# Kernel tuning notes

Measured on AMD Instinct MI355X. Metric: run time of the kernel, lower is better.

Reference implementation:

```python
import jax, jax.numpy as jnp
import numpy as np

B, SQ, SKV, D = 4, 4096, 4096, 64

def setup_inputs() -> dict:
    key = jax.random.key(0)
    kq, kv = jax.random.split(key)
    query = jax.random.normal(kq, (B, SQ, D), dtype=jnp.float32)
    value = jax.random.normal(kv, (B, SKV, D), dtype=jnp.float32)
    return {"query": query, "value": value}

def reference(query, value):
    # scores = Q @ V^T  (value acts as both keys and values; no 1/sqrt(d) scaling)
    scores = jnp.einsum('bqd,bkd->bqk', query, value)  # [B, SQ, SKV]
    dist = jax.nn.softmax(scores, axis=-1)
    context = jnp.einsum('bqk,bkd->bqd', dist, value)  # [B, SQ, D]
    return context
```

## Files before the change

### kernel.cpp

```cpp
#include <hip/hip_runtime.h>


#define NB   4
#define SQ   4096
#define SKV  4096
#define DH   64
#define L2E  1.44269504088896340736f

typedef _Float16 half8 __attribute__((ext_vector_type(8)));
typedef _Float16 half4 __attribute__((ext_vector_type(4)));
typedef _Float16 half2v __attribute__((ext_vector_type(2)));
typedef float f32x4 __attribute__((ext_vector_type(4)));
typedef unsigned short u16;

#define MFMA16(a, b, c) __builtin_amdgcn_mfma_f32_16x16x16f16((a), (b), (c), 0, 0, 0)
#define MFMA32(a, b, c) __builtin_amdgcn_mfma_f32_16x16x32_f16((a), (b), (c), 0, 0, 0)

__device__ __forceinline__ u16 f2h(float f) {
  _Float16 h = (_Float16)f;
  return __builtin_bit_cast(u16, h);
}
__device__ __forceinline__ half2v pkrtz(float a, float b) {
  return __builtin_bit_cast(half2v, __builtin_amdgcn_cvt_pkrtz(a, b));
}

typedef __attribute__((address_space(1))) void gvoid;
typedef __attribute__((address_space(3))) void lvoid;
__device__ __forceinline__ void dma16(const u16* g, u16* l) {
  __builtin_amdgcn_global_load_lds((gvoid*)g, (lvoid*)l, 16, 0, 0);
}

__global__ __launch_bounds__(256) void prep_kernel(
    const float* __restrict__ V, u16* __restrict__ vh, u16* __restrict__ vt) {
  __shared__ u16 ldsT[16 * 72];
  int blk = blockIdx.x;
  int b   = blk >> 8;
  int rem = blk & 255;
  int j0  = (rem >> 2) << 6;
  int d0  = (rem & 3) << 4;
  int t   = threadIdx.x;
  int j   = t >> 2;
  int dc  = (t & 3) << 2;

  const float* src = V + ((size_t)(b * SKV) + j0 + j) * DH + d0 + dc;
  float4 v4 = *(const float4*)src;
  u16 h[4] = {f2h(v4.x), f2h(v4.y), f2h(v4.z), f2h(v4.w)};
  unsigned p0 = (unsigned)h[0] | ((unsigned)h[1] << 16);
  unsigned p1 = (unsigned)h[2] | ((unsigned)h[3] << 16);
  int dfull = d0 + dc;
  int physd = ((((dfull >> 3) ^ (j & 7)) << 3)) + (dfull & 7);
  *(uint2*)(vh + ((size_t)(b * SKV) + j0 + j) * DH + physd) = make_uint2(p0, p1);

#pragma unroll
  for (int k = 0; k < 4; ++k) ldsT[(dc + k) * 72 + j] = h[k];
  __syncthreads();

  int dl = t >> 4;
  int jc = (t & 15) << 2;
  u16 tr[4];
#pragma unroll
  for (int k = 0; k < 4; ++k) tr[k] = ldsT[dl * 72 + jc + k];
  unsigned q0 = (unsigned)tr[0] | ((unsigned)tr[1] << 16);
  unsigned q1 = (unsigned)tr[2] | ((unsigned)tr[3] << 16);
  int d   = d0 + dl;
  int kc2 = jc >> 5;
  int g   = (jc >> 4) & 1;
  int qd  = (jc >> 2) & 3;
  int hp  = ((kc2 << 2) | qd) ^ (d & 7);
  *(uint2*)(vt + ((size_t)(b * DH) + d) * SKV + j0 + (hp << 3) + (g << 2)) =
      make_uint2(q0, q1);
}

__global__ __launch_bounds__(256, 4) void attn_kernel(
    const float* __restrict__ Q,
    const u16* __restrict__ vh,
    const u16* __restrict__ vt,
    u16* __restrict__ po,
    float* __restrict__ pm,
    float* __restrict__ pl,
    int S, int kvLen) {
  __shared__ __align__(16) u16 lds[2][2][4096];

  int blk  = blockIdx.x;
  int tile = blk / S;
  int s    = blk - tile * S;
  int b    = tile >> 6;
  int q0   = (tile & 63) << 6;
  int kv0  = s * kvLen;
  int t    = threadIdx.x;
  int wave = t >> 6;
  int lane = t & 63;
  int col  = lane & 15;
  int quad = lane >> 4;
  int qw   = q0 + (wave << 4);
  int c7   = col & 7;

  const u16* gv  = vh + (size_t)(b * SKV) * DH;
  const u16* gvt = vt + (size_t)(b * DH) * SKV;

  int r0 = t >> 3;
  int c0 = (t & 7) << 3;
  int wb = wave << 9;

  half8 qf[2];
#pragma unroll
  for (int kc = 0; kc < 2; ++kc) {
    const float* qp = Q + ((size_t)(b * SQ) + qw + col) * DH + kc * 32 + (quad << 3);
    float4 a0 = *(const float4*)qp;
    float4 a1 = *(const float4*)(qp + 4);
    half8 hq;
    hq[0] = (_Float16)(a0.x * L2E); hq[1] = (_Float16)(a0.y * L2E);
    hq[2] = (_Float16)(a0.z * L2E); hq[3] = (_Float16)(a0.w * L2E);
    hq[4] = (_Float16)(a1.x * L2E); hq[5] = (_Float16)(a1.y * L2E);
    hq[6] = (_Float16)(a1.z * L2E); hq[7] = (_Float16)(a1.w * L2E);
    qf[kc] = hq;
  }

  f32x4 o[4];
#pragma unroll
  for (int nf = 0; nf < 4; ++nf) o[nf] = (f32x4){0.f, 0.f, 0.f, 0.f};
  float m_r = -1e30f, l_r = 0.f;

  dma16(gv + ((size_t)(kv0 + r0) << 6) + c0,       &lds[0][0][0] + wb);
  dma16(gv + ((size_t)(kv0 + r0 + 32) << 6) + c0,  &lds[0][0][0] + 2048 + wb);
  dma16(gvt + (size_t)r0 * SKV + kv0 + c0,         &lds[0][1][0] + wb);
  dma16(gvt + (size_t)(r0 + 32) * SKV + kv0 + c0,  &lds[0][1][0] + 2048 + wb);

  int nIter = kvLen >> 6;
  int cur = 0;
  for (int it = 0; it < nIter; ++it) {
    __syncthreads();

    if ((it + 1) < nIter) {
      int j0n = kv0 + ((it + 1) << 6);
      u16* dv  = &lds[cur ^ 1][0][0];
      u16* dvt = &lds[cur ^ 1][1][0];
      dma16(gv + ((size_t)(j0n + r0) << 6) + c0,      dv + wb);
      dma16(gv + ((size_t)(j0n + r0 + 32) << 6) + c0, dv + 2048 + wb);
      dma16(gvt + (size_t)r0 * SKV + j0n + c0,        dvt + wb);
      dma16(gvt + (size_t)(r0 + 32) * SKV + j0n + c0, dvt + 2048 + wb);
    }

    const u16* sv = &lds[cur][0][0];
    const u16* st = &lds[cur][1][0];

    f32x4 sf[4];
#pragma unroll
    for (int nf = 0; nf < 4; ++nf) sf[nf] = (f32x4){0.f, 0.f, 0.f, 0.f};
#pragma unroll
    for (int nf = 0; nf < 4; ++nf) {
#pragma unroll
      for (int kc = 0; kc < 2; ++kc) {
        int ch = ((kc << 2) | quad) ^ c7;
        half8 av = *(const half8*)(sv + ((nf * 16 + col) << 6) + (ch << 3));
        sf[nf] = MFMA32(av, qf[kc], sf[nf]);
      }
    }

    half4 pf[4];
    {
      float tm = sf[0][0];
#pragma unroll
      for (int nf = 0; nf < 4; ++nf)
#pragma unroll
        for (int r = 0; r < 4; ++r) tm = fmaxf(tm, sf[nf][r]);
      tm = fmaxf(tm, __shfl_xor(tm, 16, 64));
      tm = fmaxf(tm, __shfl_xor(tm, 32, 64));
      float mn = fmaxf(m_r, tm);
      float al = exp2f(m_r - mn);
      m_r = mn;
      float rs = 0.f;
#pragma unroll
      for (int nf = 0; nf < 4; ++nf) {
        float p0 = exp2f(sf[nf][0] - mn);
        float p1 = exp2f(sf[nf][1] - mn);
        float p2 = exp2f(sf[nf][2] - mn);
        float p3 = exp2f(sf[nf][3] - mn);
        rs += (p0 + p1) + (p2 + p3);
        half2v lo = pkrtz(p0, p1);
        half2v hi = pkrtz(p2, p3);
        pf[nf] = __builtin_shufflevector(lo, hi, 0, 1, 2, 3);
      }
      l_r = l_r * al + rs;
#pragma unroll
      for (int nf = 0; nf < 4; ++nf)
#pragma unroll
        for (int r = 0; r < 4; ++r) o[nf][r] *= al;
    }

#pragma unroll
    for (int kc2 = 0; kc2 < 2; ++kc2) {
#pragma unroll
      for (int nf2 = 0; nf2 < 4; ++nf2) {
        int ch = ((kc2 << 2) | quad) ^ c7;
        half8 w8 = *(const half8*)(st + ((nf2 * 16 + col) << 6) + (ch << 3));
        half4 wlo = __builtin_shufflevector(w8, w8, 0, 1, 2, 3);
        half4 whi = __builtin_shufflevector(w8, w8, 4, 5, 6, 7);
        o[nf2] = MFMA16(wlo, pf[kc2 * 2], o[nf2]);
        o[nf2] = MFMA16(whi, pf[kc2 * 2 + 1], o[nf2]);
      }
    }

    cur ^= 1;
  }

  l_r += __shfl_xor(l_r, 16, 64);
  l_r += __shfl_xor(l_r, 32, 64);
  int pidx = tile * S + s;
  if (quad == 0) {
    pm[(size_t)pidx * 64 + (wave << 4) + col] = m_r;
    pl[(size_t)pidx * 64 + (wave << 4) + col] = l_r;
  }

  __syncthreads();
  u16* tp = &lds[0][0][0];
  {
    int qrow = (wave << 4) + col;
#pragma unroll
    for (int nf2 = 0; nf2 < 4; ++nf2) {
#pragma unroll
      for (int r2 = 0; r2 < 4; r2 += 2) {
        unsigned pk = (unsigned)f2h(o[nf2][r2]) |
                      ((unsigned)f2h(o[nf2][r2 + 1]) << 16);
        int d = nf2 * 16 + (quad << 2) + r2;
        *(unsigned*)(tp + qrow * 72 + d) = pk;
      }
    }
  }
  __syncthreads();
  {
    u16* pob = po + (size_t)pidx * 64 * 64;
    int q = t >> 2, hc = (t & 3) << 4;
    uint4 x0 = *(const uint4*)(tp + q * 72 + hc);
    uint4 x1 = *(const uint4*)(tp + q * 72 + hc + 8);
    *(uint4*)(pob + q * 64 + hc)     = x0;
    *(uint4*)(pob + q * 64 + hc + 8) = x1;
  }
}

__global__ __launch_bounds__(256) void combine_kernel(
    const u16* __restrict__ po,
    const float* __restrict__ pm,
    const float* __restrict__ pl,
    float* __restrict__ out, int S) {
  int t    = threadIdx.x;
  int rowg = blockIdx.x * 32 + (t >> 3);
  int tile = rowg >> 6;
  int row  = rowg & 63;
  int dc   = (t & 7) << 3;

  float mv[8], lv[8];
  float M = -1e30f;
  for (int s = 0; s < S; ++s) {
    mv[s] = pm[(size_t)(tile * S + s) * 64 + row];
    lv[s] = pl[(size_t)(tile * S + s) * 64 + row];
    M = fmaxf(M, mv[s]);
  }
  float L = 0.f, w[8];
  for (int s = 0; s < S; ++s) {
    w[s] = exp2f(mv[s] - M);
    L += lv[s] * w[s];
  }
  float acc[8] = {0.f, 0.f, 0.f, 0.f, 0.f, 0.f, 0.f, 0.f};
  for (int s = 0; s < S; ++s) {
    const u16* p = po + (size_t)(tile * S + s) * 4096 + row * 64 + dc;
    uint4 raw = *(const uint4*)p;
    half8 x = __builtin_bit_cast(half8, raw);
#pragma unroll
    for (int k = 0; k < 8; ++k) acc[k] += w[s] * (float)x[k];
  }
  float invL = 1.0f / L;
  float* op = out + (size_t)rowg * 64 + dc;
  f32x4 o0 = (f32x4){acc[0], acc[1], acc[2], acc[3]};
  f32x4 o1 = (f32x4){acc[4], acc[5], acc[6], acc[7]};
  *(f32x4*)op       = o0 * invL;
  *(f32x4*)(op + 4) = o1 * invL;
}

extern "C" void kernel_launch(void* const* d_in, const int* in_sizes, int n_in,
                              void* d_out, int out_size, void* d_ws, size_t ws_size,
                              hipStream_t stream) {
  const float* Q = (const float*)d_in[0];
  const float* V = (const float*)d_in[1];
  float* out = (float*)d_out;

  const size_t convBytes = (size_t)2 * NB * SKV * DH * 2;
  auto partBytes = [](int S) {
    return (size_t)NB * 64 * S * ((size_t)64 * 64 * 2 + 64 * 8);
  };
  int S = 4;
  while (S > 1 && ws_size < convBytes + partBytes(S)) S >>= 1;
  int kvLen = SKV / S;

  u16* vh = (u16*)d_ws;
  u16* vt = vh + (size_t)NB * SKV * DH;
  u16* po = vt + (size_t)NB * SKV * DH;
  float* pm = (float*)(po + (size_t)NB * 64 * S * 64 * 64);
  float* pl = pm + (size_t)NB * 64 * S * 64;

  prep_kernel<<<NB * 256, 256, 0, stream>>>(V, vh, vt);
  attn_kernel<<<NB * 64 * S, 256, 0, stream>>>(Q, vh, vt, po, pm, pl, S, kvLen);
  combine_kernel<<<NB * SQ / 32, 256, 0, stream>>>(po, pm, pl, out, S);
}
```

Before: 106.4 us.

## Software-pipeline PV MFMAs one iteration behind and skip redundant rescales

The P·V MFMAs are deferred by one iteration: V^T fragments and probabilities are held in registers and multiplied during the next iteration, after that iteration's QK^T MFMAs, so matrix work can overlap the softmax exponentials. The MFMA blocks are wrapped in s_setprio, the max reduction uses three-input fmax trees, and the output rescale is skipped when no lane's running max changed. The combine kernel's loops are unrolled to a fixed bound of 8 with guards. The cost is higher register pressure from holding eight half8 V fragments and the P fragments across the loop, which may lower occupancy.

```diff
diff --git a/kernel.cpp b/kernel.cpp
--- a/kernel.cpp
+++ b/kernel.cpp
@@ -22,6 +22,9 @@
 }
 __device__ __forceinline__ half2v pkrtz(float a, float b) {
   return __builtin_bit_cast(half2v, __builtin_amdgcn_cvt_pkrtz(a, b));
+}
+__device__ __forceinline__ float fmax3(float a, float b, float c) {
+  return fmaxf(fmaxf(a, b), c);
 }
 
 typedef __attribute__((address_space(1))) void gvoid;
@@ -121,6 +124,9 @@
   for (int nf = 0; nf < 4; ++nf) o[nf] = (f32x4){0.f, 0.f, 0.f, 0.f};
   float m_r = -1e30f, l_r = 0.f;
 
+  half4 pf[4];
+  half8 vr[8];
+
   dma16(gv + ((size_t)(kv0 + r0) << 6) + c0,       &lds[0][0][0] + wb);
   dma16(gv + ((size_t)(kv0 + r0 + 32) << 6) + c0,  &lds[0][0][0] + 2048 + wb);
   dma16(gvt + (size_t)r0 * SKV + kv0 + c0,         &lds[0][1][0] + wb);
@@ -147,6 +153,7 @@
     f32x4 sf[4];
 #pragma unroll
     for (int nf = 0; nf < 4; ++nf) sf[nf] = (f32x4){0.f, 0.f, 0.f, 0.f};
+    __builtin_amdgcn_s_setprio(1);
 #pragma unroll
     for (int nf = 0; nf < 4; ++nf) {
 #pragma unroll
@@ -156,19 +163,45 @@
         sf[nf] = MFMA32(av, qf[kc], sf[nf]);
       }
     }
-
-    half4 pf[4];
+    __builtin_amdgcn_s_setprio(0);
+
+    if (it > 0) {
+      __builtin_amdgcn_s_setprio(1);
+#pragma unroll
+      for (int kc2 = 0; kc2 < 2; ++kc2) {
+#pragma unroll
+        for (int nf2 = 0; nf2 < 4; ++nf2) {
+          half8 w8 = vr[kc2 * 4 + nf2];
+          half4 wlo = __builtin_shufflevector(w8, w8, 0, 1, 2, 3);
+          half4 whi = __builtin_shufflevector(w8, w8, 4, 5, 6, 7);
+          o[nf2] = MFMA16(wlo, pf[kc2 * 2], o[nf2]);
+          o[nf2] = MFMA16(whi, pf[kc2 * 2 + 1], o[nf2]);
+        }
+      }
+      __builtin_amdgcn_s_setprio(0);
+    }
+
     {
-      float tm = sf[0][0];
-#pragma unroll
-      for (int nf = 0; nf < 4; ++nf)
-#pragma unroll
-        for (int r = 0; r < 4; ++r) tm = fmaxf(tm, sf[nf][r]);
+      float t0 = fmax3(sf[0][0], sf[0][1], sf[0][2]);
+      float t1 = fmax3(sf[0][3], sf[1][0], sf[1][1]);
+      float t2 = fmax3(sf[1][2], sf[1][3], sf[2][0]);
+      float t3 = fmax3(sf[2][1], sf[2][2], sf[2][3]);
+      float t4 = fmax3(sf[3][0], sf[3][1], sf[3][2]);
+      float t5 = fmax3(t0, t1, sf[3][3]);
+      float tm = fmax3(t2, t3, t4);
+      tm = fmaxf(tm, t5);
       tm = fmaxf(tm, __shfl_xor(tm, 16, 64));
       tm = fmaxf(tm, __shfl_xor(tm, 32, 64));
       float mn = fmaxf(m_r, tm);
-      float al = exp2f(m_r - mn);
-      m_r = mn;
+      float al = 1.0f;
+      if (!__all(mn == m_r)) {
+        al = exp2f(m_r - mn);
+        m_r = mn;
+#pragma unroll
+        for (int nf = 0; nf < 4; ++nf)
+#pragma unroll
+          for (int r = 0; r < 4; ++r) o[nf][r] *= al;
+      }
       float rs = 0.f;
 #pragma unroll
       for (int nf = 0; nf < 4; ++nf) {
@@ -182,10 +215,6 @@
         pf[nf] = __builtin_shufflevector(lo, hi, 0, 1, 2, 3);
       }
       l_r = l_r * al + rs;
-#pragma unroll
-      for (int nf = 0; nf < 4; ++nf)
-#pragma unroll
-        for (int r = 0; r < 4; ++r) o[nf][r] *= al;
     }
 
 #pragma unroll
@@ -193,16 +222,26 @@
 #pragma unroll
       for (int nf2 = 0; nf2 < 4; ++nf2) {
         int ch = ((kc2 << 2) | quad) ^ c7;
-        half8 w8 = *(const half8*)(st + ((nf2 * 16 + col) << 6) + (ch << 3));
-        half4 wlo = __builtin_shufflevector(w8, w8, 0, 1, 2, 3);
-        half4 whi = __builtin_shufflevector(w8, w8, 4, 5, 6, 7);
-        o[nf2] = MFMA16(wlo, pf[kc2 * 2], o[nf2]);
-        o[nf2] = MFMA16(whi, pf[kc2 * 2 + 1], o[nf2]);
+        vr[kc2 * 4 + nf2] = *(const half8*)(st + ((nf2 * 16 + col) << 6) + (ch << 3));
       }
     }
 
     cur ^= 1;
   }
+
+  __builtin_amdgcn_s_setprio(1);
+#pragma unroll
+  for (int kc2 = 0; kc2 < 2; ++kc2) {
+#pragma unroll
+    for (int nf2 = 0; nf2 < 4; ++nf2) {
+      half8 w8 = vr[kc2 * 4 + nf2];
+      half4 wlo = __builtin_shufflevector(w8, w8, 0, 1, 2, 3);
+      half4 whi = __builtin_shufflevector(w8, w8, 4, 5, 6, 7);
+      o[nf2] = MFMA16(wlo, pf[kc2 * 2], o[nf2]);
+      o[nf2] = MFMA16(whi, pf[kc2 * 2 + 1], o[nf2]);
+    }
+  }
+  __builtin_amdgcn_s_setprio(0);
 
   l_r += __shfl_xor(l_r, 16, 64);
   l_r += __shfl_xor(l_r, 32, 64);
@@ -251,23 +290,32 @@
 
   float mv[8], lv[8];
   float M = -1e30f;
-  for (int s = 0; s < S; ++s) {
-    mv[s] = pm[(size_t)(tile * S + s) * 64 + row];
-    lv[s] = pl[(size_t)(tile * S + s) * 64 + row];
-    M = fmaxf(M, mv[s]);
+#pragma unroll
+  for (int s = 0; s < 8; ++s) {
+    if (s < S) {
+      mv[s] = pm[(size_t)(tile * S + s) * 64 + row];
+      lv[s] = pl[(size_t)(tile * S + s) * 64 + row];
+      M = fmaxf(M, mv[s]);
+    }
   }
   float L = 0.f, w[8];
-  for (int s = 0; s < S; ++s) {
-    w[s] = exp2f(mv[s] - M);
-    L += lv[s] * w[s];
+#pragma unroll
+  for (int s = 0; s < 8; ++s) {
+    if (s < S) {
+      w[s] = exp2f(mv[s] - M);
+      L += lv[s] * w[s];
+    }
   }
   float acc[8] = {0.f, 0.f, 0.f, 0.f, 0.f, 0.f, 0.f, 0.f};
-  for (int s = 0; s < S; ++s) {
-    const u16* p = po + (size_t)(tile * S + s) * 4096 + row * 64 + dc;
-    uint4 raw = *(const uint4*)p;
-    half8 x = __builtin_bit_cast(half8, raw);
-#pragma unroll
-    for (int k = 0; k < 8; ++k) acc[k] += w[s] * (float)x[k];
+#pragma unroll
+  for (int s = 0; s < 8; ++s) {
+    if (s < S) {
+      const u16* p = po + (size_t)(tile * S + s) * 4096 + row * 64 + dc;
+      uint4 raw = *(const uint4*)p;
+      half8 x = __builtin_bit_cast(half8, raw);
+#pragma unroll
+      for (int k = 0; k < 8; ++k) acc[k] += w[s] * (float)x[k];
+    }
   }
   float invL = 1.0f / L;
   float* op = out + (size_t)rowg * 64 + dc;
```

New measurement: 104.3 us (median of 2 runs). -2.0%, faster.
